# Kernel optimization log

Hardware: AMD Instinct MI355X
Metric: run time of the kernel (lower is better)

Reference implementation:

```python
import jax, jax.numpy as jnp
import numpy as np

B, C_IN, T, N = 16, 64, 12, 1024
KS, C_OUT = 3, 64


def setup_inputs() -> dict:
    key = jax.random.key(0)
    k1, k2, k3 = jax.random.split(key, 3)
    x = jax.random.normal(k1, (B, C_IN, T, N), dtype=jnp.float32)
    # graph Chebyshev kernel [N, Ks*N]; scale down so matmuls stay well-conditioned
    kernel = jax.random.normal(k2, (N, KS * N), dtype=jnp.float32) / np.sqrt(N)
    # xavier-uniform theta [Ks*c_in, c_out]
    limit = np.sqrt(6.0 / (KS * C_IN + C_OUT))
    theta = jax.random.uniform(k3, (KS * C_IN, C_OUT), dtype=jnp.float32,
                               minval=-limit, maxval=limit)
    bias = jnp.zeros((C_OUT,), dtype=jnp.float32)
    return {"x": x, "kernel": kernel, "theta": theta, "bias": bias}


def reference(x, kernel, theta, bias):
    # x: [B, C, T, N]; kernel: [N, Ks*N] viewed as [N, Ks, N]; theta: [C*Ks, c_out]
    Bb, C, Tt, Nn = x.shape
    Ks = kernel.shape[1] // Nn
    Kr = kernel.reshape(Nn, Ks, Nn)            # [n, k, m]
    th = theta.reshape(C, Ks, -1)              # [c, k, o] (row index = c*Ks + k)
    # batched spectral conv over all timesteps at once (fuses the per-t loop)
    x_mul = jnp.einsum('bctn,nkm->bctkm', x, Kr)       # [B,C,T,Ks,N]
    gc = jnp.einsum('bctkm,cko->botm', x_mul, th)      # [B,c_out,T,N]
    gc = gc + bias[None, :, None, None]
    # c_in == c_out -> residual is identity
    return jax.nn.relu(gc + x)
```

## Files before the change

kernel.cpp:

```cpp
#include <hip/hip_runtime.h>

#define NB   16
#define NC   64
#define NT   12
#define NN   1024
#define NKS  3

typedef float  f32x4  __attribute__((ext_vector_type(4)));
typedef short  s16x8  __attribute__((ext_vector_type(8)));
typedef unsigned short u16x4 __attribute__((ext_vector_type(4)));
typedef unsigned short u16x8 __attribute__((ext_vector_type(8)));
typedef unsigned short ush;

__device__ __forceinline__ ush f2bf(float f) {
    union { float f; unsigned u; } v; v.f = f;
    unsigned r = v.u + 0x7FFFu + ((v.u >> 16) & 1u);
    return (ush)(r >> 16);
}
__device__ __forceinline__ float bf2f(ush h) {
    union { unsigned u; float f; } v; v.u = ((unsigned)h) << 16;
    return v.f;
}

__device__ __forceinline__ void cp16(const void* g, void* l) {
    __builtin_amdgcn_global_load_lds(
        (const __attribute__((address_space(1))) unsigned int*)g,
        (__attribute__((address_space(3))) unsigned int*)l, 16, 0, 0);
}

#define APAN_OFF 0
#define KB_OFF   25165824
#define TH_OFF   31457280

__global__ __launch_bounds__(256)
void spatio_prep(const float* __restrict__ x, const float* __restrict__ kern,
                 const float* __restrict__ theta,
                 ush* __restrict__ apan, ush* __restrict__ kb, ush* __restrict__ thbf)
{
    const int blk = blockIdx.x;
    const int tid = threadIdx.x;

    if (blk < 1536) {
        int ch   = blk * 256 + tid;
        int j    = ch % 192;
        int rest = ch / 192;
        int d    = rest & 3;
        int nb   = (rest >> 2) & 31;
        int mt   = rest >> 7;
        int k    = j >> 6, mm = j & 63;
        int col  = (k << 10) + (mt << 6) + mm;
        u16x8 w;
#pragma unroll
        for (int i = 0; i < 8; ++i) {
            int n = nb * 32 + d * 8 + i;
            w[i] = f2bf(kern[(size_t)n * (NKS * NN) + col]);
        }
        size_t base = ((size_t)(mt * 32 + nb) * 768) + j * 4 + (d ^ (j & 3));
        ((u16x8*)kb)[base] = w;
    } else if (blk < 1584) {
        int id = (blk - 1536) * 256 + tid;
        if (id < 12288) {
            int row = id >> 6, o = id & 63;
            int c = row / 3, k = row - 3 * c;
            thbf[o * 192 + k * 64 + c] = f2bf(theta[id]);
        }
    } else {
        int id   = (blk - 1584) * 256 + tid;
        int slot = id & 511;
        int g2nb = id >> 9;
        int nb   = g2nb & 31, g2 = g2nb >> 5;
        int row  = slot >> 2, p = slot & 3;
        int d    = p ^ (row & 3);
        int bl   = row >> 6, c = row & 63;
        int bt   = 2 * g2 + bl;
        int b    = bt / NT, t = bt - NT * b;
        const float* src = x + ((size_t)((b * NC + c) * NT + t)) * NN + nb * 32 + d * 8;
        float4 a0 = ((const float4*)src)[0];
        float4 a1 = ((const float4*)src)[1];
        u16x8 w;
        w[0] = f2bf(a0.x); w[1] = f2bf(a0.y); w[2] = f2bf(a0.z); w[3] = f2bf(a0.w);
        w[4] = f2bf(a1.x); w[5] = f2bf(a1.y); w[6] = f2bf(a1.z); w[7] = f2bf(a1.w);
        ((u16x8*)apan)[id] = w;
    }
}

__global__ __launch_bounds__(256, 2)
void spatio_main(const ush* __restrict__ apan, const ush* __restrict__ kb,
                 const ush* __restrict__ thbf, const float* __restrict__ bias,
                 float* __restrict__ out)
{
    __shared__ __attribute__((aligned(128))) char smem[41984];
    ush (*As)[32]  = (ush (*)[32])smem;
    ush (*Bs)[32]  = (ush (*)[32])(smem + 8192);
    ush (*xm)[200] = (ush (*)[200])smem;
    ush (*stL)[32] = (ush (*)[32])(smem + 25600);
    ush (*stH)[32] = (ush (*)[32])(smem + 33792);

    const int tid  = threadIdx.x;
    const int g2   = blockIdx.x;
    const int mt   = blockIdx.y;
    const int m_base = mt * 64;
    const int lane = tid & 63;
    const int wid  = tid >> 6;
    const int wr   = wid & 1;
    const int wn   = wid >> 1;
    const int quad = lane >> 4;
    const int l16  = lane & 15;
    const int pofs = (quad ^ (l16 & 3)) * 8;

    const char* apan_c = (const char*)apan + ((size_t)g2 << 18);
    const char* kb_c   = (const char*)kb + ((size_t)mt * 32 * 768 * 16);

    f32x4 acc[4][6];
#pragma unroll
    for (int i = 0; i < 4; ++i)
#pragma unroll
        for (int j = 0; j < 6; ++j) acc[i][j] = (f32x4){0.f, 0.f, 0.f, 0.f};

    for (int it = 0; it < 32; ++it) {
        __syncthreads();
        const char* asrc = apan_c + ((size_t)it << 13);
        const char* bsrc = kb_c + ((size_t)it * 12288);
#pragma unroll
        for (int i = 0; i < 2; ++i)
            cp16(asrc + (i * 256 + tid) * 16, smem + (i * 256 + tid) * 16);
#pragma unroll
        for (int i = 0; i < 3; ++i)
            cp16(bsrc + (i * 256 + tid) * 16, smem + 8192 + (i * 256 + tid) * 16);
        if ((it >> 1) == mt) {
            char* sb = smem + 25600 + (it & 1) * 8192;
#pragma unroll
            for (int i = 0; i < 2; ++i) {
                int m = i * 256 + tid;
                int slot = (m & ~3) + ((m & 3) ^ ((m >> 2) & 3));
                cp16(asrc + slot * 16, sb + m * 16);
            }
        }
        __syncthreads();

        s16x8 af[4], bf[6];
#pragma unroll
        for (int rb = 0; rb < 4; ++rb)
            af[rb] = *(const s16x8*)&As[64 * wr + 16 * rb + l16][pofs];
#pragma unroll
        for (int jb = 0; jb < 6; ++jb)
            bf[jb] = *(const s16x8*)&Bs[96 * wn + 16 * jb + l16][pofs];
#pragma unroll
        for (int rb = 0; rb < 4; ++rb)
#pragma unroll
            for (int jb = 0; jb < 6; ++jb)
                acc[rb][jb] = __builtin_amdgcn_mfma_f32_16x16x32_bf16(af[rb], bf[jb], acc[rb][jb], 0, 0, 0);
    }

    float bo[4];
#pragma unroll
    for (int r = 0; r < 4; ++r) bo[r] = bias[16 * wid + 4 * quad + r];

    for (int pass = 0; pass < 2; ++pass) {
        __syncthreads();
        if (wr == pass) {
#pragma unroll
            for (int rb = 0; rb < 4; ++rb)
#pragma unroll
                for (int jb = 0; jb < 6; ++jb) {
                    int J  = 96 * wn + 16 * jb + l16;
                    int kk = J >> 6, mm = J & 63;
                    int ck0 = kk * 64 + 16 * rb + 4 * quad;
                    u16x4 w;
                    w.x = f2bf(acc[rb][jb].x); w.y = f2bf(acc[rb][jb].y);
                    w.z = f2bf(acc[rb][jb].z); w.w = f2bf(acc[rb][jb].w);
                    *(u16x4*)&xm[mm][ck0] = w;
                }
        }
        __syncthreads();

        f32x4 acc2[4];
#pragma unroll
        for (int jb = 0; jb < 4; ++jb) acc2[jb] = (f32x4){0.f, 0.f, 0.f, 0.f};
#pragma unroll
        for (int ks = 0; ks < 6; ++ks) {
            s16x8 a2 = *(const s16x8*)(thbf + (size_t)(16 * wid + l16) * 192 + ks * 32 + quad * 8);
#pragma unroll
            for (int jb = 0; jb < 4; ++jb) {
                s16x8 b2 = *(const s16x8*)&xm[16 * jb + l16][ks * 32 + quad * 8];
                acc2[jb] = __builtin_amdgcn_mfma_f32_16x16x32_bf16(a2, b2, acc2[jb], 0, 0, 0);
            }
        }

        const int bt = 2 * g2 + pass;
        const int b2i = bt / NT, t2 = bt - NT * b2i;
#pragma unroll
        for (int jb = 0; jb < 4; ++jb) {
            int mm = 16 * jb + l16;
#pragma unroll
            for (int r = 0; r < 4; ++r) {
                int o = 16 * wid + 4 * quad + r;
                int row = pass * 64 + o;
                ush rv = (jb < 2) ? stL[row][mm] : stH[row][mm - 32];
                size_t idx = (((size_t)(b2i * NC + o) * NT + t2) * NN) + m_base + mm;
                float v = acc2[jb][r] + bo[r] + bf2f(rv);
                out[idx] = fmaxf(v, 0.f);
            }
        }
    }
}

extern "C" void kernel_launch(void* const* d_in, const int* in_sizes, int n_in,
                              void* d_out, int out_size, void* d_ws, size_t ws_size,
                              hipStream_t stream) {
    const float* x     = (const float*)d_in[0];
    const float* kern  = (const float*)d_in[1];
    const float* theta = (const float*)d_in[2];
    const float* bias  = (const float*)d_in[3];
    float* out = (float*)d_out;
    (void)in_sizes; (void)n_in; (void)out_size; (void)ws_size;

    ush* apan = (ush*)((char*)d_ws + APAN_OFF);
    ush* kbp  = (ush*)((char*)d_ws + KB_OFF);
    ush* thbf = (ush*)((char*)d_ws + TH_OFF);

    hipLaunchKernelGGL(spatio_prep, dim3(7728), dim3(256), 0, stream,
                       x, kern, theta, apan, kbp, thbf);
    hipLaunchKernelGGL(spatio_main, dim3(96, 16), dim3(256), 0, stream,
                       apan, kbp, thbf, bias, out);
}
```

Baseline: 188.6 us.

## Double-buffer LDS tiles in main GEMM loop and coalesce kernel-panel writes

The main loop now keeps two LDS buffers: it prefetches the next A/B k-tile while computing on the current one, which removes one barrier per iteration and hides global-to-LDS latency. LDS use grows to 57 KB per block, and the residual staging area moves to make room. The prep kernel now picks its source indices from the output slot, so kernel-panel stores are contiguous while keeping the same swizzled layout. Whether the overlap actually happens depends on the compiler not inserting a full vmcnt wait before the LDS reads.

Result: no change. 186.3 us (-1.2%).

```diff
diff --git a/kernel.cpp b/kernel.cpp
--- a/kernel.cpp
+++ b/kernel.cpp
@@ -42,11 +42,11 @@
 
     if (blk < 1536) {
         int ch   = blk * 256 + tid;
-        int j    = ch % 192;
-        int rest = ch / 192;
-        int d    = rest & 3;
-        int nb   = (rest >> 2) & 31;
-        int mt   = rest >> 7;
+        int p    = ch & 3;
+        int j    = (ch >> 2) % 192;
+        int rest = (ch >> 2) / 192;
+        int nb   = rest & 31, mt = rest >> 5;
+        int d    = p ^ (j & 3);
         int k    = j >> 6, mm = j & 63;
         int col  = (k << 10) + (mt << 6) + mm;
         u16x8 w;
@@ -55,8 +55,7 @@
             int n = nb * 32 + d * 8 + i;
             w[i] = f2bf(kern[(size_t)n * (NKS * NN) + col]);
         }
-        size_t base = ((size_t)(mt * 32 + nb) * 768) + j * 4 + (d ^ (j & 3));
-        ((u16x8*)kb)[base] = w;
+        ((u16x8*)kb)[ch] = w;
     } else if (blk < 1584) {
         int id = (blk - 1536) * 256 + tid;
         if (id < 12288) {
@@ -89,12 +88,10 @@
                  const ush* __restrict__ thbf, const float* __restrict__ bias,
                  float* __restrict__ out)
 {
-    __shared__ __attribute__((aligned(128))) char smem[41984];
-    ush (*As)[32]  = (ush (*)[32])smem;
-    ush (*Bs)[32]  = (ush (*)[32])(smem + 8192);
+    __shared__ __attribute__((aligned(128))) char smem[57344];
     ush (*xm)[200] = (ush (*)[200])smem;
-    ush (*stL)[32] = (ush (*)[32])(smem + 25600);
-    ush (*stH)[32] = (ush (*)[32])(smem + 33792);
+    ush (*stL)[32] = (ush (*)[32])(smem + 40960);
+    ush (*stH)[32] = (ush (*)[32])(smem + 49152);
 
     const int tid  = threadIdx.x;
     const int g2   = blockIdx.x;
@@ -117,18 +114,31 @@
 #pragma unroll
         for (int j = 0; j < 6; ++j) acc[i][j] = (f32x4){0.f, 0.f, 0.f, 0.f};
 
+#pragma unroll
+    for (int i = 0; i < 2; ++i)
+        cp16(apan_c + (i * 256 + tid) * 16, smem + (i * 256 + tid) * 16);
+#pragma unroll
+    for (int i = 0; i < 3; ++i)
+        cp16(kb_c + (i * 256 + tid) * 16, smem + 8192 + (i * 256 + tid) * 16);
+
     for (int it = 0; it < 32; ++it) {
+        const int p = it & 1;
+        char* buf = smem + p * 20480;
         __syncthreads();
-        const char* asrc = apan_c + ((size_t)it << 13);
-        const char* bsrc = kb_c + ((size_t)it * 12288);
-#pragma unroll
-        for (int i = 0; i < 2; ++i)
-            cp16(asrc + (i * 256 + tid) * 16, smem + (i * 256 + tid) * 16);
-#pragma unroll
-        for (int i = 0; i < 3; ++i)
-            cp16(bsrc + (i * 256 + tid) * 16, smem + 8192 + (i * 256 + tid) * 16);
+        if (it < 31) {
+            const char* asrc = apan_c + ((size_t)(it + 1) << 13);
+            const char* bsrc = kb_c + (size_t)(it + 1) * 12288;
+            char* nbuf = smem + (p ^ 1) * 20480;
+#pragma unroll
+            for (int i = 0; i < 2; ++i)
+                cp16(asrc + (i * 256 + tid) * 16, nbuf + (i * 256 + tid) * 16);
+#pragma unroll
+            for (int i = 0; i < 3; ++i)
+                cp16(bsrc + (i * 256 + tid) * 16, nbuf + 8192 + (i * 256 + tid) * 16);
+        }
         if ((it >> 1) == mt) {
-            char* sb = smem + 25600 + (it & 1) * 8192;
+            const char* asrc = apan_c + ((size_t)it << 13);
+            char* sb = smem + 40960 + (it & 1) * 8192;
 #pragma unroll
             for (int i = 0; i < 2; ++i) {
                 int m = i * 256 + tid;
@@ -136,8 +146,9 @@
                 cp16(asrc + slot * 16, sb + m * 16);
             }
         }
-        __syncthreads();
-
+
+        ush (*As)[32] = (ush (*)[32])buf;
+        ush (*Bs)[32] = (ush (*)[32])(buf + 8192);
         s16x8 af[4], bf[6];
 #pragma unroll
         for (int rb = 0; rb < 4; ++rb)
```
